# Performance work log

Measured on AMD Instinct MI355X. Metric: run time of the kernel, lower is better.

Reference implementation:

```python
import jax, jax.numpy as jnp
import numpy as np

DIM = 192
WINDOW_SIZE = 8
NUM_HEADS = 6
HEAD_DIM = DIM // NUM_HEADS
SCALE = HEAD_DIM ** (-0.5)
META_HIDDEN = 256


def get_relative_positions(window_size):
    coords = np.stack(np.meshgrid(np.arange(window_size), np.arange(window_size), indexing='ij'))  # [2, ws, ws]
    coords_flatten = coords.reshape(2, -1)  # [2, N]
    rel = coords_flatten[:, :, None] - coords_flatten[:, None, :]  # [2, N, N]
    rel = np.transpose(rel, (1, 2, 0)).astype(np.float32)  # [N, N, 2]
    return np.sign(rel) * np.log1p(np.abs(rel))


def setup_inputs() -> dict:
    key = jax.random.key(0)
    k_qkv, k_w1, k_b1, k_w2, k_b2 = jax.random.split(key, 5)
    B_, N = 2048, WINDOW_SIZE * WINDOW_SIZE
    qkv = jax.random.normal(k_qkv, (B_, N, 3 * DIM), dtype=jnp.float32)
    # meta MLP: Linear(2, 256) -> ReLU -> Linear(256, num_heads)
    w1 = jax.random.normal(k_w1, (2, META_HIDDEN), dtype=jnp.float32) * (1.0 / np.sqrt(2.0))
    b1 = jax.random.normal(k_b1, (META_HIDDEN,), dtype=jnp.float32) * 0.01
    w2 = jax.random.normal(k_w2, (META_HIDDEN, NUM_HEADS), dtype=jnp.float32) * (1.0 / np.sqrt(META_HIDDEN))
    b2 = jax.random.normal(k_b2, (NUM_HEADS,), dtype=jnp.float32) * 0.01
    rel_pos = jnp.asarray(get_relative_positions(WINDOW_SIZE))  # [N, N, 2]
    return {"qkv": qkv, "rel_pos": rel_pos, "w1": w1, "b1": b1, "w2": w2, "b2": b2}


def reference(qkv, rel_pos, w1, b1, w2, b2):
    B_, N, _ = qkv.shape
    qkv = qkv.reshape(B_, N, 3, NUM_HEADS, HEAD_DIM).transpose(2, 0, 3, 1, 4)  # [3, B, H, N, hd]
    q, k, v = qkv[0], qkv[1], qkv[2]
    attn = jnp.einsum('bhnd,bhmd->bhnm', q * SCALE, k)  # [B, H, N, N]
    # relative-position bias via small MLP: [N, N, 2] -> [N, N, H]
    bias = jax.nn.relu(rel_pos @ w1 + b1) @ w2 + b2
    bias = bias.transpose(2, 0, 1)  # [H, N, N]
    attn = jax.nn.softmax(attn + bias[None], axis=-1)
    x = jnp.einsum('bhnm,bhmd->bhnd', attn, v)  # [B, H, N, hd]
    return x.transpose(0, 2, 1, 3).reshape(B_, N, DIM)
```

## Files before the change

### kernel.cpp

```cpp
#include <hip/hip_runtime.h>
#include <hip/hip_bf16.h>

#define NHEADS 6
#define HDIM 32
#define NTOK 64
#define QK_LD 40
#define VT_LD 72
#define P_LD 72

typedef short short8v __attribute__((ext_vector_type(8)));
typedef short short4v __attribute__((ext_vector_type(4)));
typedef float float4v __attribute__((ext_vector_type(4)));

__device__ __forceinline__ short f2bf(float f) {
    union { __hip_bfloat16 h; short s; } u;
    u.h = __float2bfloat16(f);
    return u.s;
}

__global__ void bias_mlp_kernel(const float* __restrict__ rel_pos,
                                const float* __restrict__ w1,
                                const float* __restrict__ b1,
                                const float* __restrict__ w2,
                                const float* __restrict__ b2,
                                float* __restrict__ bias) {
    int idx = blockIdx.x * blockDim.x + threadIdx.x;
    float r0 = rel_pos[idx * 2 + 0];
    float r1 = rel_pos[idx * 2 + 1];
    float acc[NHEADS];
#pragma unroll
    for (int h = 0; h < NHEADS; ++h) acc[h] = b2[h];
    for (int j = 0; j < 256; ++j) {
        float hv = fmaf(r0, w1[j], fmaf(r1, w1[256 + j], b1[j]));
        hv = fmaxf(hv, 0.0f);
#pragma unroll
        for (int h = 0; h < NHEADS; ++h)
            acc[h] = fmaf(hv, w2[j * NHEADS + h], acc[h]);
    }
#pragma unroll
    for (int h = 0; h < NHEADS; ++h)
        bias[h * 4096 + idx] = acc[h];
}

__global__ __launch_bounds__(256, 3)
void attn_kernel(const float* __restrict__ qkv,
                 const float* __restrict__ bias,
                 float* __restrict__ out) {
    __shared__ short s_q[2][NTOK][QK_LD];
    __shared__ short s_k[2][NTOK][QK_LD];
    __shared__ short s_vt[2][HDIM][VT_LD];
    __shared__ short s_p[2][NTOK][P_LD];

    const int tid = threadIdx.x;
    const int b = blockIdx.x;
    const int h0 = blockIdx.y * 2;
    const float* base = qkv + (size_t)b * (NTOK * 576);

#pragma unroll
    for (int it = 0; it < 12; ++it) {
        int idx = tid + it * 256;
        int row = idx / 48;
        int cc = idx - row * 48;
        int chunk = cc >> 3;
        int part = chunk >> 1;
        int hsel = chunk & 1;
        int d = (cc & 7) * 4;
        float4v v4 = *(const float4v*)(base + row * 576 + part * 192 + (h0 + hsel) * 32 + d);
        if (part == 0) {
            const float s = 0.17677669529663687f;
            short4v pk;
            pk.x = f2bf(v4.x * s); pk.y = f2bf(v4.y * s);
            pk.z = f2bf(v4.z * s); pk.w = f2bf(v4.w * s);
            *(short4v*)&s_q[hsel][row][d] = pk;
        } else if (part == 1) {
            short4v pk;
            pk.x = f2bf(v4.x); pk.y = f2bf(v4.y);
            pk.z = f2bf(v4.z); pk.w = f2bf(v4.w);
            *(short4v*)&s_k[hsel][row][d] = pk;
        } else {
            s_vt[hsel][d + 0][row] = f2bf(v4.x);
            s_vt[hsel][d + 1][row] = f2bf(v4.y);
            s_vt[hsel][d + 2][row] = f2bf(v4.z);
            s_vt[hsel][d + 3][row] = f2bf(v4.w);
        }
    }
    __syncthreads();

    const int wid = tid >> 6;
    const int lane = tid & 63;
    const int hl = wid >> 1;
    const int half = wid & 1;
    const int c = lane & 15;
    const int quad = lane >> 4;
    const int rbase = half * 32;

    short8v aq[2], bk[4];
#pragma unroll
    for (int i = 0; i < 2; ++i)
        aq[i] = *(const short8v*)&s_q[hl][rbase + i * 16 + c][quad * 8];
#pragma unroll
    for (int j = 0; j < 4; ++j)
        bk[j] = *(const short8v*)&s_k[hl][j * 16 + c][quad * 8];

    float4v S[2][4];
#pragma unroll
    for (int i = 0; i < 2; ++i)
#pragma unroll
        for (int j = 0; j < 4; ++j) {
            float4v z = {0.f, 0.f, 0.f, 0.f};
            S[i][j] = __builtin_amdgcn_mfma_f32_16x16x32_bf16(aq[i], bk[j], z, 0, 0, 0);
        }

    const float* bh = bias + (h0 + hl) * 4096;
    float rs[2][4];
#pragma unroll
    for (int i = 0; i < 2; ++i) {
#pragma unroll
        for (int r = 0; r < 4; ++r) {
            int row = rbase + i * 16 + quad * 4 + r;
            const float* brow = bh + row * 64 + c;
            float l0 = S[i][0][r] + brow[0];
            float l1 = S[i][1][r] + brow[16];
            float l2 = S[i][2][r] + brow[32];
            float l3 = S[i][3][r] + brow[48];
            float m = fmaxf(fmaxf(l0, l1), fmaxf(l2, l3));
#pragma unroll
            for (int off = 1; off < 16; off <<= 1)
                m = fmaxf(m, __shfl_xor(m, off, 64));
            l0 = __expf(l0 - m); l1 = __expf(l1 - m);
            l2 = __expf(l2 - m); l3 = __expf(l3 - m);
            float sum = l0 + l1 + l2 + l3;
#pragma unroll
            for (int off = 1; off < 16; off <<= 1)
                sum += __shfl_xor(sum, off, 64);
            rs[i][r] = 1.0f / sum;
            s_p[hl][row][c]      = f2bf(l0);
            s_p[hl][row][c + 16] = f2bf(l1);
            s_p[hl][row][c + 32] = f2bf(l2);
            s_p[hl][row][c + 48] = f2bf(l3);
        }
    }

    short8v bv[2][2], pa[2][2];
#pragma unroll
    for (int t = 0; t < 2; ++t)
#pragma unroll
        for (int kk = 0; kk < 2; ++kk)
            bv[t][kk] = *(const short8v*)&s_vt[hl][t * 16 + c][kk * 32 + quad * 8];
#pragma unroll
    for (int i = 0; i < 2; ++i)
#pragma unroll
        for (int kk = 0; kk < 2; ++kk)
            pa[i][kk] = *(const short8v*)&s_p[hl][rbase + i * 16 + c][kk * 32 + quad * 8];

    float4v O[2][2];
#pragma unroll
    for (int i = 0; i < 2; ++i)
#pragma unroll
        for (int t = 0; t < 2; ++t) {
            float4v z = {0.f, 0.f, 0.f, 0.f};
            z = __builtin_amdgcn_mfma_f32_16x16x32_bf16(pa[i][0], bv[t][0], z, 0, 0, 0);
            O[i][t] = __builtin_amdgcn_mfma_f32_16x16x32_bf16(pa[i][1], bv[t][1], z, 0, 0, 0);
        }

    float* ob = out + (size_t)b * (NTOK * 192) + (h0 + hl) * 32;
#pragma unroll
    for (int i = 0; i < 2; ++i)
#pragma unroll
        for (int t = 0; t < 2; ++t)
#pragma unroll
            for (int r = 0; r < 4; ++r) {
                int row = rbase + i * 16 + quad * 4 + r;
                ob[row * 192 + t * 16 + c] = O[i][t][r] * rs[i][r];
            }
}

extern "C" void kernel_launch(void* const* d_in, const int* in_sizes, int n_in,
                              void* d_out, int out_size, void* d_ws, size_t ws_size,
                              hipStream_t stream) {
    const float* qkv     = (const float*)d_in[0];
    const float* rel_pos = (const float*)d_in[1];
    const float* w1      = (const float*)d_in[2];
    const float* b1      = (const float*)d_in[3];
    const float* w2      = (const float*)d_in[4];
    const float* b2      = (const float*)d_in[5];
    float* bias = (float*)d_ws;
    float* out  = (float*)d_out;

    bias_mlp_kernel<<<dim3(64), dim3(64), 0, stream>>>(rel_pos, w1, b1, w2, b2, bias);
    attn_kernel<<<dim3(2048, 3), dim3(256), 0, stream>>>(qkv, bias, out);
}
```

Baseline: 487.5 us.

## Transpose score MFMA, alias P over Q/K in LDS, raise occupancy

Computes S^T by swapping MFMA operands so each lane holds a full query row slice, which cuts the softmax reductions to two cross-quad shuffles and allows vectorized float4 bias loads and packed short4 P stores. Normalization is folded into P before the PV matmul, so the output store no longer rescales. The P buffer aliases the Q/K LDS region behind an added barrier, shrinking shared memory so launch bounds can ask for 4 blocks per CU. This adds one __syncthreads and may increase register pressure under the tighter occupancy target.

```diff
diff --git a/kernel.cpp b/kernel.cpp
--- a/kernel.cpp
+++ b/kernel.cpp
@@ -2,7 +2,6 @@
 #include <hip/hip_bf16.h>
 
 #define NHEADS 6
-#define HDIM 32
 #define NTOK 64
 #define QK_LD 40
 #define VT_LD 72
@@ -42,14 +41,15 @@
         bias[h * 4096 + idx] = acc[h];
 }
 
-__global__ __launch_bounds__(256, 3)
+__global__ __launch_bounds__(256, 4)
 void attn_kernel(const float* __restrict__ qkv,
                  const float* __restrict__ bias,
                  float* __restrict__ out) {
-    __shared__ short s_q[2][NTOK][QK_LD];
-    __shared__ short s_k[2][NTOK][QK_LD];
-    __shared__ short s_vt[2][HDIM][VT_LD];
-    __shared__ short s_p[2][NTOK][P_LD];
+    __shared__ __align__(16) char s_qkp[20480];
+    __shared__ __align__(16) short s_vt[2][32][VT_LD];
+    short (*s_q)[NTOK][QK_LD] = (short (*)[NTOK][QK_LD])(s_qkp);
+    short (*s_k)[NTOK][QK_LD] = (short (*)[NTOK][QK_LD])(s_qkp + 10240);
+    short (*s_p)[NTOK][P_LD]  = (short (*)[NTOK][P_LD])(s_qkp);
 
     const int tid = threadIdx.x;
     const int b = blockIdx.x;
@@ -68,14 +68,10 @@
         float4v v4 = *(const float4v*)(base + row * 576 + part * 192 + (h0 + hsel) * 32 + d);
         if (part == 0) {
             const float s = 0.17677669529663687f;
-            short4v pk;
-            pk.x = f2bf(v4.x * s); pk.y = f2bf(v4.y * s);
-            pk.z = f2bf(v4.z * s); pk.w = f2bf(v4.w * s);
+            short4v pk = { f2bf(v4.x * s), f2bf(v4.y * s), f2bf(v4.z * s), f2bf(v4.w * s) };
             *(short4v*)&s_q[hsel][row][d] = pk;
         } else if (part == 1) {
-            short4v pk;
-            pk.x = f2bf(v4.x); pk.y = f2bf(v4.y);
-            pk.z = f2bf(v4.z); pk.w = f2bf(v4.w);
+            short4v pk = { f2bf(v4.x), f2bf(v4.y), f2bf(v4.z), f2bf(v4.w) };
             *(short4v*)&s_k[hsel][row][d] = pk;
         } else {
             s_vt[hsel][d + 0][row] = f2bf(v4.x);
@@ -102,42 +98,50 @@
     for (int j = 0; j < 4; ++j)
         bk[j] = *(const short8v*)&s_k[hl][j * 16 + c][quad * 8];
 
-    float4v S[2][4];
+    float4v T[4][2];
 #pragma unroll
-    for (int i = 0; i < 2; ++i)
+    for (int j = 0; j < 4; ++j)
+#pragma unroll
+        for (int i = 0; i < 2; ++i) {
+            float4v z = {0.f, 0.f, 0.f, 0.f};
+            T[j][i] = __builtin_amdgcn_mfma_f32_16x16x32_bf16(bk[j], aq[i], z, 0, 0, 0);
+        }
+
+    __syncthreads();
+
+    const float* bh = bias + (h0 + hl) * 4096;
+#pragma unroll
+    for (int i = 0; i < 2; ++i) {
+        const int qrow = rbase + i * 16 + c;
+        float L[4][4];
+        float m = -1e30f;
 #pragma unroll
         for (int j = 0; j < 4; ++j) {
-            float4v z = {0.f, 0.f, 0.f, 0.f};
-            S[i][j] = __builtin_amdgcn_mfma_f32_16x16x32_bf16(aq[i], bk[j], z, 0, 0, 0);
+            float4v bb = *(const float4v*)(bh + qrow * 64 + j * 16 + quad * 4);
+#pragma unroll
+            for (int r = 0; r < 4; ++r) {
+                L[j][r] = T[j][i][r] + bb[r];
+                m = fmaxf(m, L[j][r]);
+            }
         }
-
-    const float* bh = bias + (h0 + hl) * 4096;
-    float rs[2][4];
+        m = fmaxf(m, __shfl_xor(m, 16, 64));
+        m = fmaxf(m, __shfl_xor(m, 32, 64));
+        float sum = 0.f;
 #pragma unroll
-    for (int i = 0; i < 2; ++i) {
+        for (int j = 0; j < 4; ++j)
 #pragma unroll
-        for (int r = 0; r < 4; ++r) {
-            int row = rbase + i * 16 + quad * 4 + r;
-            const float* brow = bh + row * 64 + c;
-            float l0 = S[i][0][r] + brow[0];
-            float l1 = S[i][1][r] + brow[16];
-            float l2 = S[i][2][r] + brow[32];
-            float l3 = S[i][3][r] + brow[48];
-            float m = fmaxf(fmaxf(l0, l1), fmaxf(l2, l3));
+            for (int r = 0; r < 4; ++r) {
+                L[j][r] = __expf(L[j][r] - m);
+                sum += L[j][r];
+            }
+        sum += __shfl_xor(sum, 16, 64);
+        sum += __shfl_xor(sum, 32, 64);
+        float inv = 1.0f / sum;
 #pragma unroll
-            for (int off = 1; off < 16; off <<= 1)
-                m = fmaxf(m, __shfl_xor(m, off, 64));
-            l0 = __expf(l0 - m); l1 = __expf(l1 - m);
-            l2 = __expf(l2 - m); l3 = __expf(l3 - m);
-            float sum = l0 + l1 + l2 + l3;
-#pragma unroll
-            for (int off = 1; off < 16; off <<= 1)
-                sum += __shfl_xor(sum, off, 64);
-            rs[i][r] = 1.0f / sum;
-            s_p[hl][row][c]      = f2bf(l0);
-            s_p[hl][row][c + 16] = f2bf(l1);
-            s_p[hl][row][c + 32] = f2bf(l2);
-            s_p[hl][row][c + 48] = f2bf(l3);
+        for (int j = 0; j < 4; ++j) {
+            short4v pk = { f2bf(L[j][0] * inv), f2bf(L[j][1] * inv),
+                           f2bf(L[j][2] * inv), f2bf(L[j][3] * inv) };
+            *(short4v*)&s_p[hl][qrow][j * 16 + quad * 4] = pk;
         }
     }
 
@@ -171,7 +175,7 @@
 #pragma unroll
             for (int r = 0; r < 4; ++r) {
                 int row = rbase + i * 16 + quad * 4 + r;
-                ob[row * 192 + t * 16 + c] = O[i][t][r] * rs[i][r];
+                ob[row * 192 + t * 16 + c] = O[i][t][r];
             }
 }
 
```

Result: no change. 478.9 us (-1.8%).
